# Kernel tuning notes

Measured on AMD Instinct MI355X. Metric: run time of the kernel, lower is better.

The kernel has to match this reference:

```python
import jax, jax.numpy as jnp
import numpy as np

NUM_EVENT, EVENT_DIM = 6, 32
NUM_WORD, WORD_DIM = 100000, 128
NUM_SKU, SKU_DIM = 500000, 128
NUM_CAT, CAT_DIM = 10000, 64
NUM_PRICE, PRICE_DIM = 100, 32
NUM_URL, URL_DIM = 200000, 128
HIDDEN = 512
B, S, W = 256, 256, 12
PAD = 0


def _table(key, n, d):
    t = jax.random.normal(key, (n, d), dtype=jnp.float32) * 0.02
    return t.at[PAD].set(0.0)  # padding_idx row is zero


def setup_inputs() -> dict:
    key = jax.random.key(0)
    ks = jax.random.split(key, 20)
    inp = {
        "event_table": _table(ks[0], NUM_EVENT, EVENT_DIM),
        "word_table": _table(ks[1], NUM_WORD, WORD_DIM),
        "sku_table": _table(ks[2], NUM_SKU, SKU_DIM),
        "cat_table": _table(ks[3], NUM_CAT, CAT_DIM),
        "price_table": _table(ks[4], NUM_PRICE, PRICE_DIM),
        "url_table": _table(ks[5], NUM_URL, URL_DIM),
        # Linear weights, torch convention: y = x @ W.T + b
        "sku_w": jax.random.normal(ks[6], (HIDDEN, EVENT_DIM + SKU_DIM + CAT_DIM + PRICE_DIM + WORD_DIM), dtype=jnp.float32) * 0.02,
        "sku_b": jnp.zeros((HIDDEN,), dtype=jnp.float32),
        "url_w": jax.random.normal(ks[7], (HIDDEN, URL_DIM + EVENT_DIM), dtype=jnp.float32) * 0.02,
        "url_b": jnp.zeros((HIDDEN,), dtype=jnp.float32),
        "query_w": jax.random.normal(ks[8], (HIDDEN, EVENT_DIM + WORD_DIM), dtype=jnp.float32) * 0.02,
        "query_b": jnp.zeros((HIDDEN,), dtype=jnp.float32),
        "event_type": jax.random.randint(ks[9], (B, S), 0, NUM_EVENT, dtype=jnp.int32),
        "sku_id": jax.random.randint(ks[10], (B, S), 0, NUM_SKU, dtype=jnp.int32),
        "url_id": jax.random.randint(ks[11], (B, S), 0, NUM_URL, dtype=jnp.int32),
        "cat_id": jax.random.randint(ks[12], (B, S), 0, NUM_CAT, dtype=jnp.int32),
        "price_id": jax.random.randint(ks[13], (B, S), 0, NUM_PRICE, dtype=jnp.int32),
        "word_id": jax.random.randint(ks[14], (B, S, W), 0, NUM_WORD, dtype=jnp.int32),
    }
    return inp


def _linear_relu(x, w, b):
    return jax.nn.relu(jnp.einsum("bsi,hi->bsh", x, w) + b)


def reference(event_table, word_table, sku_table, cat_table, price_table, url_table,
              sku_w, sku_b, url_w, url_b, query_w, query_b,
              event_type, sku_id, url_id, cat_id, price_id, word_id):
    # padding mask: 1.0 where event_type == PAD_IDX
    src_padding_mask = (event_type == PAD).astype(jnp.float32)

    event_emb = event_table[event_type]                 # [B,S,E]
    word_emb = word_table[word_id].mean(axis=-2)        # [B,S,Wd] (WordEmbedding avg)

    # SKU branch (event types 1,2,3): concat(event, sku, cat, price, word)
    sku_in = jnp.concatenate([event_emb, sku_table[sku_id], cat_table[cat_id],
                              price_table[price_id], word_emb], axis=-1)
    sku_out = _linear_relu(sku_in, sku_w, sku_b)        # [B,S,H]

    # URL branch (event type 4): concat(url, event)  -- note order in UrlEmbedding
    url_in = jnp.concatenate([url_table[url_id], event_emb], axis=-1)
    url_out = _linear_relu(url_in, url_w, url_b)

    # Query branch (event type 5): concat(event, word)
    query_in = jnp.concatenate([event_emb, word_emb], axis=-1)
    query_out = _linear_relu(query_in, query_w, query_b)

    is_sku = ((event_type >= 1) & (event_type <= 3))[..., None]
    is_url = (event_type == 4)[..., None]
    is_query = (event_type == 5)[..., None]

    seq_emb = (jnp.where(is_sku, sku_out, 0.0)
               + jnp.where(is_url, url_out, 0.0)
               + jnp.where(is_query, query_out, 0.0))   # PAD positions stay zero
    return seq_emb, src_padding_mask
```

## Files before the change

### kernel.cpp

```cpp
#include <hip/hip_runtime.h>
#include <hip/hip_bf16.h>
#if !__has_builtin(__builtin_amdgcn_cvt_pk_fp8_f32) || !__has_builtin(__builtin_amdgcn_cvt_pk_f32_fp8)
#include <hip/hip_fp8.h>
#endif

#define CUR_OFF   0
#define SLOT_OFF  1024
#define POS_OFF   263168
#define WSKU_OFF  1049600
#define WURL_OFF  1246208
#define WQRY_OFF  1344512
#define WF8_OFF   2097152
#define XS_OFF    16777216
#define XU_OFF    50331648
#define XQ_OFF    68157440

#define NPOS      65536
#define OUT_MASK  33554432
#define F8_SCALE  64.0f
#define INV4096   (1.0f / 4096.0f)

typedef __attribute__((ext_vector_type(4))) float f32x4;
typedef __attribute__((ext_vector_type(2))) float f32x2;
typedef __attribute__((ext_vector_type(2))) unsigned int u32x2;

__device__ __forceinline__ float2 ld2(const float* p) {
    return *reinterpret_cast<const float2*>(p);
}

__device__ __forceinline__ unsigned int pk2_f8(float a, float b) {
#if __has_builtin(__builtin_amdgcn_cvt_pk_fp8_f32)
    return __builtin_amdgcn_cvt_pk_fp8_f32(a, b, 0u, false);
#else
    __hip_fp8_e4m3 fa(a), fb(b);
    return (unsigned int)fa.__x | ((unsigned int)fb.__x << 8);
#endif
}
__device__ __forceinline__ unsigned int pk4_f8(float a, float b, float c, float d) {
#if __has_builtin(__builtin_amdgcn_cvt_pk_fp8_f32)
    unsigned int v = 0;
    v = __builtin_amdgcn_cvt_pk_fp8_f32(a, b, v, false);
    v = __builtin_amdgcn_cvt_pk_fp8_f32(c, d, v, true);
    return v;
#else
    return pk2_f8(a, b) | (pk2_f8(c, d) << 16);
#endif
}
__device__ __forceinline__ float2 upk2_f8(unsigned int u) {
#if __has_builtin(__builtin_amdgcn_cvt_pk_f32_fp8)
    f32x2 r = __builtin_amdgcn_cvt_pk_f32_fp8(u, false);
    return make_float2(r.x, r.y);
#else
    __hip_fp8_e4m3 fa, fb;
    fa.__x = (unsigned char)(u & 0xff);
    fb.__x = (unsigned char)((u >> 8) & 0xff);
    return make_float2((float)fa, (float)fb);
#endif
}
__device__ __forceinline__ void st_f8x2(unsigned char* d, float a, float b) {
    *reinterpret_cast<unsigned short*>(d) = (unsigned short)(pk2_f8(a, b) & 0xffffu);
}

#define AS1(p) ((const __attribute__((address_space(1))) void*)(p))
#define AS3(p) ((__attribute__((address_space(3))) void*)(p))

__global__ __launch_bounds__(256) void prep_k(const float* __restrict__ sw,
                                              const float* __restrict__ uw,
                                              const float* __restrict__ qw,
                                              const float* __restrict__ word_t,
                                              char* ws) {
    const int b = blockIdx.x, t = threadIdx.x;
    if (b < 6250) {
        size_t i = ((size_t)b * 256 + t) * 8;
        f32x4 v0 = *reinterpret_cast<const f32x4*>(word_t + i);
        f32x4 v1 = *reinterpret_cast<const f32x4*>(word_t + i + 4);
        u32x2 pk;
        pk.x = pk4_f8(v0.x * F8_SCALE, v0.y * F8_SCALE, v0.z * F8_SCALE, v0.w * F8_SCALE);
        pk.y = pk4_f8(v1.x * F8_SCALE, v1.y * F8_SCALE, v1.z * F8_SCALE, v1.w * F8_SCALE);
        *reinterpret_cast<u32x2*>((unsigned char*)(ws + WF8_OFF) + i) = pk;
        return;
    }
    int tt = (b - 6250) * 256 + t;
    if (tt < 3) ((int*)(ws + CUR_OFF))[tt] = 0;
    if (tt < 196608) {
        ((unsigned char*)(ws + WSKU_OFF))[tt] =
            (unsigned char)(pk2_f8(sw[tt] * F8_SCALE, 0.f) & 0xffu);
    } else if (tt < 294912) {
        int i = tt - 196608; int n = i / 192, k = i % 192;
        ((unsigned char*)(ws + WURL_OFF))[i] = (k < 160)
            ? (unsigned char)(pk2_f8(uw[n * 160 + k] * F8_SCALE, 0.f) & 0xffu) : 0;
    } else {
        int i = tt - 294912; int n = i / 192, k = i % 192;
        ((unsigned char*)(ws + WQRY_OFF))[i] = (k < 160)
            ? (unsigned char)(pk2_f8(qw[n * 160 + k] * F8_SCALE, 0.f) & 0xffu) : 0;
    }
}

__global__ __launch_bounds__(256) void alloc_k(const int* __restrict__ et_a,
                                               float* __restrict__ out, char* ws) {
    __shared__ int s_wcnt[4][3];
    __shared__ int s_base[3];
    __shared__ int s_woff[4][3];
    const int t = threadIdx.x, lane = t & 63, wid = t >> 6;
    int p = blockIdx.x * 256 + t;
    int et = et_a[p];
    int br = (et >= 1 && et <= 3) ? 0 : (et == 4 ? 1 : (et == 5 ? 2 : -1));
    unsigned long long m0 = __ballot(br == 0);
    unsigned long long m1 = __ballot(br == 1);
    unsigned long long m2 = __ballot(br == 2);
    if (lane == 0) {
        s_wcnt[wid][0] = (int)__popcll(m0);
        s_wcnt[wid][1] = (int)__popcll(m1);
        s_wcnt[wid][2] = (int)__popcll(m2);
    }
    __syncthreads();
    if (t < 3) {
        int c0 = s_wcnt[0][t], c1 = s_wcnt[1][t], c2 = s_wcnt[2][t], c3 = s_wcnt[3][t];
        int tot = c0 + c1 + c2 + c3;
        s_base[t] = tot ? atomicAdd(&((int*)(ws + CUR_OFF))[t], tot) : 0;
        s_woff[0][t] = 0; s_woff[1][t] = c0; s_woff[2][t] = c0 + c1; s_woff[3][t] = c0 + c1 + c2;
    }
    __syncthreads();
    unsigned long long lt = (1ull << lane) - 1ull;
    int slot = -1;
    if (br == 0)      slot = s_base[0] + s_woff[wid][0] + (int)__popcll(m0 & lt);
    else if (br == 1) slot = s_base[1] + s_woff[wid][1] + (int)__popcll(m1 & lt);
    else if (br == 2) slot = s_base[2] + s_woff[wid][2] + (int)__popcll(m2 & lt);
    ((int*)(ws + SLOT_OFF))[p] = slot;
    if (slot >= 0) ((int*)(ws + POS_OFF))[br * NPOS + slot] = p;
    __builtin_nontemporal_store((et == 0) ? 1.0f : 0.0f, &out[OUT_MASK + p]);
}

__device__ __forceinline__ float2 wsum_f8(const unsigned char* __restrict__ wt8,
                                          const int* __restrict__ wids, int lane) {
    float sx = 0.f, sy = 0.f;
    #pragma unroll
    for (int k = 0; k < 12; ++k) {
        unsigned int u = *reinterpret_cast<const unsigned short*>(
            wt8 + (size_t)wids[k] * 128 + 2 * lane);
        float2 v = upk2_f8(u);
        sx += v.x; sy += v.y;
    }
    const float inv = 1.0f / 12.0f;
    return make_float2(sx * inv, sy * inv);
}

__global__ __launch_bounds__(256) void build_k(
    const float* __restrict__ ev_t,
    const float* __restrict__ sku_t,  const float* __restrict__ cat_t,
    const float* __restrict__ price_t,const float* __restrict__ url_t,
    const int* __restrict__ et_a,     const int* __restrict__ sku_id,
    const int* __restrict__ url_id,   const int* __restrict__ cat_id,
    const int* __restrict__ price_id, const int* __restrict__ word_id,
    float* __restrict__ out, char* ws)
{
    const int t = threadIdx.x, lane = t & 63, wid = t >> 6;
    const int p = blockIdx.x * 4 + wid;
    const int et = et_a[p];
    if (et == 0) {
        f32x4 z = {0.f, 0.f, 0.f, 0.f};
        float* orow = out + (size_t)p * 512;
        __builtin_nontemporal_store(z, reinterpret_cast<f32x4*>(&orow[lane * 8]));
        __builtin_nontemporal_store(z, reinterpret_cast<f32x4*>(&orow[lane * 8 + 4]));
        return;
    }
    const int slot = ((const int*)(ws + SLOT_OFF))[p];
    const unsigned char* wf8 = (const unsigned char*)(ws + WF8_OFF);
    const float* evr = ev_t + et * 32;
    if (et <= 3) {
        unsigned char* X = (unsigned char*)(ws + XS_OFF) + (size_t)slot * 384;
        if (lane < 16) { float2 e = ld2(evr + 2 * lane);
                         st_f8x2(X + 2 * lane, e.x * F8_SCALE, e.y * F8_SCALE); }
        const float* sr = sku_t + (size_t)sku_id[p] * 128;
        { float2 s = ld2(sr + 2 * lane);
          st_f8x2(X + 32 + 2 * lane, s.x * F8_SCALE, s.y * F8_SCALE); }
        if (lane < 32) { const float* cr = cat_t + (size_t)cat_id[p] * 64;
                         float2 c = ld2(cr + 2 * lane);
                         st_f8x2(X + 160 + 2 * lane, c.x * F8_SCALE, c.y * F8_SCALE); }
        if (lane < 16) { const float* pr = price_t + (size_t)price_id[p] * 32;
                         float2 v = ld2(pr + 2 * lane);
                         st_f8x2(X + 224 + 2 * lane, v.x * F8_SCALE, v.y * F8_SCALE); }
        float2 w = wsum_f8(wf8, word_id + (size_t)p * 12, lane);
        st_f8x2(X + 256 + 2 * lane, w.x, w.y);
    } else if (et == 4) {
        unsigned char* X = (unsigned char*)(ws + XU_OFF) + (size_t)slot * 192;
        const float* ur = url_t + (size_t)url_id[p] * 128;
        { float2 u = ld2(ur + 2 * lane);
          st_f8x2(X + 2 * lane, u.x * F8_SCALE, u.y * F8_SCALE); }
        if (lane < 16) { float2 e = ld2(evr + 2 * lane);
                         st_f8x2(X + 128 + 2 * lane, e.x * F8_SCALE, e.y * F8_SCALE); }
        if (lane >= 48) *reinterpret_cast<unsigned short*>(X + 160 + 2 * (lane - 48)) = 0;
    } else {
        unsigned char* X = (unsigned char*)(ws + XQ_OFF) + (size_t)slot * 192;
        if (lane < 16) { float2 e = ld2(evr + 2 * lane);
                         st_f8x2(X + 2 * lane, e.x * F8_SCALE, e.y * F8_SCALE); }
        float2 w = wsum_f8(wf8, word_id + (size_t)p * 12, lane);
        st_f8x2(X + 32 + 2 * lane, w.x, w.y);
        if (lane >= 48) *reinterpret_cast<unsigned short*>(X + 160 + 2 * (lane - 48)) = 0;
    }
}

__global__ __launch_bounds__(256, 2) void gemm2_k(
    const char* __restrict__ ws_c, const float* __restrict__ sku_b,
    const float* __restrict__ url_b, const float* __restrict__ qry_b,
    float* __restrict__ out)
{
    const int z = blockIdx.z;
    const int count = ((const int*)(ws_c + CUR_OFF))[z];
    const int nmt = (count + 127) >> 7;
    const int orig = blockIdx.x;
    if (orig >= nmt) return;
    const int q8 = nmt >> 3, r8 = nmt & 7;
    const int xcd = orig & 7, idx = orig >> 3;
    const int mt = (xcd < r8 ? xcd * (q8 + 1) : r8 * (q8 + 1) + (xcd - r8) * q8) + idx;
    const int row0 = mt * 128;

    const int* posm = (const int*)(ws_c + POS_OFF) + z * NPOS;
    const char* arena; const char* Wb; const float* bias; int astride;
    if (z == 0)      { arena = ws_c + XS_OFF; Wb = ws_c + WSKU_OFF; bias = sku_b; astride = 384; }
    else if (z == 1) { arena = ws_c + XU_OFF; Wb = ws_c + WURL_OFF; bias = url_b; astride = 192; }
    else             { arena = ws_c + XQ_OFF; Wb = ws_c + WQRY_OFF; bias = qry_b; astride = 192; }

    __shared__ char ldsA[49152];
    __shared__ char ldsB[2][16384];

    const int t = threadIdx.x, lane = t & 63, wid = t >> 6;
    const int wr = wid >> 1, wc = wid & 1;
    const int r = lane & 15, q = lane >> 4;

    auto stageA_full = [&](int ktA, int koff) {
        #pragma unroll
        for (int i = 0; i < 4; ++i) {
            int row = i * 32 + (t >> 3);
            int sb  = (t & 7) ^ (row & 7);
            const char* ga = arena + (size_t)(row0 + row) * astride + koff + sb * 16;
            __builtin_amdgcn_global_load_lds(AS1(ga), AS3(&ldsA[ktA * 16384 + i * 4096 + t * 16]), 16, 0, 0);
        }
    };
    auto stageA_half = [&](int koff) {
        #pragma unroll
        for (int i = 0; i < 2; ++i) {
            int row = i * 64 + (t >> 2);
            int sb  = (t & 3) ^ (row & 3);
            const char* ga = arena + (size_t)(row0 + row) * astride + koff + sb * 16;
            __builtin_amdgcn_global_load_lds(AS1(ga), AS3(&ldsA[16384 + i * 4096 + t * 16]), 16, 0, 0);
        }
    };
    auto stageB_full = [&](int buf, int nc, int koff) {
        #pragma unroll
        for (int i = 0; i < 4; ++i) {
            int row = i * 32 + (t >> 3);
            int sb  = (t & 7) ^ (row & 7);
            const char* gb = Wb + (size_t)(nc * 128 + row) * astride + koff + sb * 16;
            __builtin_amdgcn_global_load_lds(AS1(gb), AS3(&ldsB[buf][i * 4096 + t * 16]), 16, 0, 0);
        }
    };
    auto stageB_half = [&](int buf, int nc, int koff) {
        #pragma unroll
        for (int i = 0; i < 2; ++i) {
            int row = i * 64 + (t >> 2);
            int sb  = (t & 3) ^ (row & 3);
            const char* gb = Wb + (size_t)(nc * 128 + row) * astride + koff + sb * 16;
            __builtin_amdgcn_global_load_lds(AS1(gb), AS3(&ldsB[buf][i * 4096 + t * 16]), 16, 0, 0);
        }
    };

    if (z == 0) { stageA_full(0, 0); stageA_full(1, 128); stageA_full(2, 256); }
    else        { stageA_full(0, 0); stageA_half(128); }
    stageB_full(0, 0, 0);
    if (z == 0) stageB_full(1, 0, 128); else stageB_half(1, 0, 128);
    __syncthreads();

    int posr[16];
    #pragma unroll
    for (int m = 0; m < 4; ++m)
        #pragma unroll
        for (int j = 0; j < 4; ++j) {
            int gr = row0 + wr * 64 + m * 16 + q * 4 + j;
            posr[m * 4 + j] = (gr < count) ? posm[gr] : -1;
        }

    f32x4 acc[4][4];
    auto compA_full = [&](int ktA, int buf) {
        #pragma unroll
        for (int kk = 0; kk < 4; ++kk) {
            const int u  = kk * 2 + (q >> 1);
            const int wo = (q & 1) * 8;
            long af[4], bf[4];
            #pragma unroll
            for (int m = 0; m < 4; ++m) {
                int arow = wr * 64 + m * 16 + r;
                af[m] = *reinterpret_cast<const long*>(
                    &ldsA[ktA * 16384 + arow * 128 + ((u ^ (arow & 7)) << 4) + wo]);
            }
            #pragma unroll
            for (int n = 0; n < 4; ++n) {
                int brow = wc * 64 + n * 16 + r;
                bf[n] = *reinterpret_cast<const long*>(
                    &ldsB[buf][brow * 128 + ((u ^ (brow & 7)) << 4) + wo]);
            }
            #pragma unroll
            for (int m = 0; m < 4; ++m)
                #pragma unroll
                for (int n = 0; n < 4; ++n)
                    acc[m][n] = __builtin_amdgcn_mfma_f32_16x16x32_fp8_fp8(af[m], bf[n], acc[m][n], 0, 0, 0);
        }
    };
    auto compA_half = [&](int buf) {
        #pragma unroll
        for (int kk = 0; kk < 2; ++kk) {
            const int u  = kk * 2 + (q >> 1);
            const int wo = (q & 1) * 8;
            long af[4], bf[4];
            #pragma unroll
            for (int m = 0; m < 4; ++m) {
                int arow = wr * 64 + m * 16 + r;
                af[m] = *reinterpret_cast<const long*>(
                    &ldsA[16384 + arow * 64 + ((u ^ (arow & 3)) << 4) + wo]);
            }
            #pragma unroll
            for (int n = 0; n < 4; ++n) {
                int brow = wc * 64 + n * 16 + r;
                bf[n] = *reinterpret_cast<const long*>(
                    &ldsB[buf][brow * 64 + ((u ^ (brow & 3)) << 4) + wo]);
            }
            #pragma unroll
            for (int m = 0; m < 4; ++m)
                #pragma unroll
                for (int n = 0; n < 4; ++n)
                    acc[m][n] = __builtin_amdgcn_mfma_f32_16x16x32_fp8_fp8(af[m], bf[n], acc[m][n], 0, 0, 0);
        }
    };
    auto epilogue = [&](int nc) {
        float bv[4];
        #pragma unroll
        for (int n = 0; n < 4; ++n) bv[n] = bias[nc * 128 + wc * 64 + n * 16 + r];
        #pragma unroll
        for (int m = 0; m < 4; ++m)
            #pragma unroll
            for (int j = 0; j < 4; ++j) {
                int pos = posr[m * 4 + j];
                if (pos >= 0) {
                    float* orow = out + (size_t)pos * 512 + nc * 128 + wc * 64;
                    #pragma unroll
                    for (int n = 0; n < 4; ++n)
                        __builtin_nontemporal_store(
                            fmaxf(acc[m][n][j] * INV4096 + bv[n], 0.f), &orow[n * 16 + r]);
                }
            }
    };

    if (z == 0) {
        for (int nc = 0; nc < 4; ++nc) {
            #pragma unroll
            for (int m = 0; m < 4; ++m)
                #pragma unroll
                for (int n = 0; n < 4; ++n)
                    acc[m][n] = (f32x4){0.f, 0.f, 0.f, 0.f};
            #pragma unroll
            for (int kt = 0; kt < 3; ++kt) {
                int j = nc * 3 + kt, jn = j + 1;
                if (jn < 12) stageB_full(jn & 1, jn / 3, (jn % 3) * 128);
                compA_full(kt, j & 1);
                __syncthreads();
            }
            epilogue(nc);
        }
    } else {
        for (int nc = 0; nc < 4; ++nc) {
            #pragma unroll
            for (int m = 0; m < 4; ++m)
                #pragma unroll
                for (int n = 0; n < 4; ++n)
                    acc[m][n] = (f32x4){0.f, 0.f, 0.f, 0.f};
            #pragma unroll
            for (int kt = 0; kt < 2; ++kt) {
                int j = nc * 2 + kt, jn = j + 1;
                if (jn < 8) {
                    if ((jn & 1) == 0) stageB_full(jn & 1, jn / 2, 0);
                    else               stageB_half(jn & 1, jn / 2, 128);
                }
                if (kt == 0) compA_full(0, j & 1);
                else         compA_half(j & 1);
                __syncthreads();
            }
            epilogue(nc);
        }
    }
}

extern "C" void kernel_launch(void* const* d_in, const int* in_sizes, int n_in,
                              void* d_out, int out_size, void* d_ws, size_t ws_size,
                              hipStream_t stream) {
    const float* ev_t    = (const float*)d_in[0];
    const float* word_t  = (const float*)d_in[1];
    const float* sku_t   = (const float*)d_in[2];
    const float* cat_t   = (const float*)d_in[3];
    const float* price_t = (const float*)d_in[4];
    const float* url_t   = (const float*)d_in[5];
    const float* sku_w   = (const float*)d_in[6];
    const float* sku_b   = (const float*)d_in[7];
    const float* url_w   = (const float*)d_in[8];
    const float* url_b   = (const float*)d_in[9];
    const float* query_w = (const float*)d_in[10];
    const float* query_b = (const float*)d_in[11];
    const int* event_type = (const int*)d_in[12];
    const int* sku_id     = (const int*)d_in[13];
    const int* url_id     = (const int*)d_in[14];
    const int* cat_id     = (const int*)d_in[15];
    const int* price_id   = (const int*)d_in[16];
    const int* word_id    = (const int*)d_in[17];

    char*  ws  = (char*)d_ws;
    float* out = (float*)d_out;

    prep_k<<<7786, 256, 0, stream>>>(sku_w, url_w, query_w, word_t, ws);
    alloc_k<<<256, 256, 0, stream>>>(event_type, out, ws);
    build_k<<<16384, 256, 0, stream>>>(ev_t, sku_t, cat_t, price_t, url_t,
                                       event_type, sku_id, url_id, cat_id, price_id,
                                       word_id, out, ws);
    dim3 gg(512, 1, 3);
    gemm2_k<<<gg, 256, 0, stream>>>(ws, sku_b, url_b, query_b, out);
}
```

Measured before the change: 87.00 us.

## Restructure gather kernel per branch with 16 lanes per row and wide loads

Result: faster. 76.39 us, median of 2 (-12.2%).

```diff
diff --git a/kernel.cpp b/kernel.cpp
--- a/kernel.cpp
+++ b/kernel.cpp
@@ -55,6 +55,14 @@
     fa.__x = (unsigned char)(u & 0xff);
     fb.__x = (unsigned char)((u >> 8) & 0xff);
     return make_float2((float)fa, (float)fb);
+#endif
+}
+__device__ __forceinline__ float2 upk2_f8_hi(unsigned int u) {
+#if __has_builtin(__builtin_amdgcn_cvt_pk_f32_fp8)
+    f32x2 r = __builtin_amdgcn_cvt_pk_f32_fp8(u, true);
+    return make_float2(r.x, r.y);
+#else
+    return upk2_f8(u >> 16);
 #endif
 }
 __device__ __forceinline__ void st_f8x2(unsigned char* d, float a, float b) {
@@ -101,9 +109,12 @@
     __shared__ int s_wcnt[4][3];
     __shared__ int s_base[3];
     __shared__ int s_woff[4][3];
+    __shared__ int s_et[256];
     const int t = threadIdx.x, lane = t & 63, wid = t >> 6;
-    int p = blockIdx.x * 256 + t;
+    const int p0 = blockIdx.x * 256;
+    int p = p0 + t;
     int et = et_a[p];
+    s_et[t] = et;
     int br = (et >= 1 && et <= 3) ? 0 : (et == 4 ? 1 : (et == 5 ? 2 : -1));
     unsigned long long m0 = __ballot(br == 0);
     unsigned long long m1 = __ballot(br == 1);
@@ -126,23 +137,30 @@
     if (br == 0)      slot = s_base[0] + s_woff[wid][0] + (int)__popcll(m0 & lt);
     else if (br == 1) slot = s_base[1] + s_woff[wid][1] + (int)__popcll(m1 & lt);
     else if (br == 2) slot = s_base[2] + s_woff[wid][2] + (int)__popcll(m2 & lt);
-    ((int*)(ws + SLOT_OFF))[p] = slot;
     if (slot >= 0) ((int*)(ws + POS_OFF))[br * NPOS + slot] = p;
     __builtin_nontemporal_store((et == 0) ? 1.0f : 0.0f, &out[OUT_MASK + p]);
-}
-
-__device__ __forceinline__ float2 wsum_f8(const unsigned char* __restrict__ wt8,
-                                          const int* __restrict__ wids, int lane) {
-    float sx = 0.f, sy = 0.f;
+    for (int i = wid; i < 256; i += 4) {
+        if (s_et[i] == 0) {
+            float* orow = out + (size_t)(p0 + i) * 512;
+            f32x4 z = {0.f, 0.f, 0.f, 0.f};
+            __builtin_nontemporal_store(z, reinterpret_cast<f32x4*>(&orow[lane * 8]));
+            __builtin_nontemporal_store(z, reinterpret_cast<f32x4*>(&orow[lane * 8 + 4]));
+        }
+    }
+}
+
+__device__ __forceinline__ void wsum8_f8(const unsigned char* __restrict__ wt8,
+                                         const int* __restrict__ wid_p, int l,
+                                         float* s) {
     #pragma unroll
     for (int k = 0; k < 12; ++k) {
-        unsigned int u = *reinterpret_cast<const unsigned short*>(
-            wt8 + (size_t)wids[k] * 128 + 2 * lane);
-        float2 v = upk2_f8(u);
-        sx += v.x; sy += v.y;
-    }
-    const float inv = 1.0f / 12.0f;
-    return make_float2(sx * inv, sy * inv);
+        int w = wid_p[k];
+        u32x2 u = *reinterpret_cast<const u32x2*>(wt8 + (size_t)w * 128 + 8 * l);
+        float2 a0 = upk2_f8(u.x), a1 = upk2_f8_hi(u.x);
+        float2 b0 = upk2_f8(u.y), b1 = upk2_f8_hi(u.y);
+        s[0] += a0.x; s[1] += a0.y; s[2] += a1.x; s[3] += a1.y;
+        s[4] += b0.x; s[5] += b0.y; s[6] += b1.x; s[7] += b1.y;
+    }
 }
 
 __global__ __launch_bounds__(256) void build_k(
@@ -152,51 +170,66 @@
     const int* __restrict__ et_a,     const int* __restrict__ sku_id,
     const int* __restrict__ url_id,   const int* __restrict__ cat_id,
     const int* __restrict__ price_id, const int* __restrict__ word_id,
-    float* __restrict__ out, char* ws)
+    char* ws)
 {
+    const int z = blockIdx.z;
+    const int count = ((const int*)(ws + CUR_OFF))[z];
+    const int slot0 = blockIdx.x * 16;
+    if (slot0 >= count) return;
     const int t = threadIdx.x, lane = t & 63, wid = t >> 6;
-    const int p = blockIdx.x * 4 + wid;
-    const int et = et_a[p];
-    if (et == 0) {
-        f32x4 z = {0.f, 0.f, 0.f, 0.f};
-        float* orow = out + (size_t)p * 512;
-        __builtin_nontemporal_store(z, reinterpret_cast<f32x4*>(&orow[lane * 8]));
-        __builtin_nontemporal_store(z, reinterpret_cast<f32x4*>(&orow[lane * 8 + 4]));
-        return;
-    }
-    const int slot = ((const int*)(ws + SLOT_OFF))[p];
+    const int g = lane >> 4, l = lane & 15;
+    const int slot = slot0 + wid * 4 + g;
+    if (slot >= count) return;
+    const int p = ((const int*)(ws + POS_OFF))[z * NPOS + slot];
     const unsigned char* wf8 = (const unsigned char*)(ws + WF8_OFF);
-    const float* evr = ev_t + et * 32;
-    if (et <= 3) {
+    const float inv = 1.0f / 12.0f;
+
+    if (z == 0) {
         unsigned char* X = (unsigned char*)(ws + XS_OFF) + (size_t)slot * 384;
-        if (lane < 16) { float2 e = ld2(evr + 2 * lane);
-                         st_f8x2(X + 2 * lane, e.x * F8_SCALE, e.y * F8_SCALE); }
-        const float* sr = sku_t + (size_t)sku_id[p] * 128;
-        { float2 s = ld2(sr + 2 * lane);
-          st_f8x2(X + 32 + 2 * lane, s.x * F8_SCALE, s.y * F8_SCALE); }
-        if (lane < 32) { const float* cr = cat_t + (size_t)cat_id[p] * 64;
-                         float2 c = ld2(cr + 2 * lane);
-                         st_f8x2(X + 160 + 2 * lane, c.x * F8_SCALE, c.y * F8_SCALE); }
-        if (lane < 16) { const float* pr = price_t + (size_t)price_id[p] * 32;
-                         float2 v = ld2(pr + 2 * lane);
-                         st_f8x2(X + 224 + 2 * lane, v.x * F8_SCALE, v.y * F8_SCALE); }
-        float2 w = wsum_f8(wf8, word_id + (size_t)p * 12, lane);
-        st_f8x2(X + 256 + 2 * lane, w.x, w.y);
-    } else if (et == 4) {
+        const int et = et_a[p];
+        float2 e = ld2(ev_t + et * 32 + 2 * l);
+        st_f8x2(X + 2 * l, e.x * F8_SCALE, e.y * F8_SCALE);
+        const float* sr = sku_t + (size_t)sku_id[p] * 128 + 8 * l;
+        f32x4 s0 = *reinterpret_cast<const f32x4*>(sr);
+        f32x4 s1 = *reinterpret_cast<const f32x4*>(sr + 4);
+        u32x2 sp;
+        sp.x = pk4_f8(s0.x * F8_SCALE, s0.y * F8_SCALE, s0.z * F8_SCALE, s0.w * F8_SCALE);
+        sp.y = pk4_f8(s1.x * F8_SCALE, s1.y * F8_SCALE, s1.z * F8_SCALE, s1.w * F8_SCALE);
+        *reinterpret_cast<u32x2*>(X + 32 + 8 * l) = sp;
+        f32x4 c = *reinterpret_cast<const f32x4*>(cat_t + (size_t)cat_id[p] * 64 + 4 * l);
+        *reinterpret_cast<unsigned int*>(X + 160 + 4 * l) =
+            pk4_f8(c.x * F8_SCALE, c.y * F8_SCALE, c.z * F8_SCALE, c.w * F8_SCALE);
+        float2 v = ld2(price_t + (size_t)price_id[p] * 32 + 2 * l);
+        st_f8x2(X + 224 + 2 * l, v.x * F8_SCALE, v.y * F8_SCALE);
+        float s[8] = {0.f, 0.f, 0.f, 0.f, 0.f, 0.f, 0.f, 0.f};
+        wsum8_f8(wf8, word_id + (size_t)p * 12, l, s);
+        u32x2 wp;
+        wp.x = pk4_f8(s[0] * inv, s[1] * inv, s[2] * inv, s[3] * inv);
+        wp.y = pk4_f8(s[4] * inv, s[5] * inv, s[6] * inv, s[7] * inv);
+        *reinterpret_cast<u32x2*>(X + 256 + 8 * l) = wp;
+    } else if (z == 1) {
         unsigned char* X = (unsigned char*)(ws + XU_OFF) + (size_t)slot * 192;
-        const float* ur = url_t + (size_t)url_id[p] * 128;
-        { float2 u = ld2(ur + 2 * lane);
-          st_f8x2(X + 2 * lane, u.x * F8_SCALE, u.y * F8_SCALE); }
-        if (lane < 16) { float2 e = ld2(evr + 2 * lane);
-                         st_f8x2(X + 128 + 2 * lane, e.x * F8_SCALE, e.y * F8_SCALE); }
-        if (lane >= 48) *reinterpret_cast<unsigned short*>(X + 160 + 2 * (lane - 48)) = 0;
+        const float* ur = url_t + (size_t)url_id[p] * 128 + 8 * l;
+        f32x4 u0 = *reinterpret_cast<const f32x4*>(ur);
+        f32x4 u1 = *reinterpret_cast<const f32x4*>(ur + 4);
+        u32x2 up;
+        up.x = pk4_f8(u0.x * F8_SCALE, u0.y * F8_SCALE, u0.z * F8_SCALE, u0.w * F8_SCALE);
+        up.y = pk4_f8(u1.x * F8_SCALE, u1.y * F8_SCALE, u1.z * F8_SCALE, u1.w * F8_SCALE);
+        *reinterpret_cast<u32x2*>(X + 8 * l) = up;
+        float2 e = ld2(ev_t + 4 * 32 + 2 * l);
+        st_f8x2(X + 128 + 2 * l, e.x * F8_SCALE, e.y * F8_SCALE);
+        *reinterpret_cast<unsigned short*>(X + 160 + 2 * l) = 0;
     } else {
         unsigned char* X = (unsigned char*)(ws + XQ_OFF) + (size_t)slot * 192;
-        if (lane < 16) { float2 e = ld2(evr + 2 * lane);
-                         st_f8x2(X + 2 * lane, e.x * F8_SCALE, e.y * F8_SCALE); }
-        float2 w = wsum_f8(wf8, word_id + (size_t)p * 12, lane);
-        st_f8x2(X + 32 + 2 * lane, w.x, w.y);
-        if (lane >= 48) *reinterpret_cast<unsigned short*>(X + 160 + 2 * (lane - 48)) = 0;
+        float2 e = ld2(ev_t + 5 * 32 + 2 * l);
+        st_f8x2(X + 2 * l, e.x * F8_SCALE, e.y * F8_SCALE);
+        float s[8] = {0.f, 0.f, 0.f, 0.f, 0.f, 0.f, 0.f, 0.f};
+        wsum8_f8(wf8, word_id + (size_t)p * 12, l, s);
+        u32x2 wp;
+        wp.x = pk4_f8(s[0] * inv, s[1] * inv, s[2] * inv, s[3] * inv);
+        wp.y = pk4_f8(s[4] * inv, s[5] * inv, s[6] * inv, s[7] * inv);
+        *reinterpret_cast<u32x2*>(X + 32 + 8 * l) = wp;
+        *reinterpret_cast<unsigned short*>(X + 160 + 2 * l) = 0;
     }
 }
 
@@ -416,9 +449,10 @@
 
     prep_k<<<7786, 256, 0, stream>>>(sku_w, url_w, query_w, word_t, ws);
     alloc_k<<<256, 256, 0, stream>>>(event_type, out, ws);
-    build_k<<<16384, 256, 0, stream>>>(ev_t, sku_t, cat_t, price_t, url_t,
-                                       event_type, sku_id, url_id, cat_id, price_id,
-                                       word_id, out, ws);
+    dim3 gb(4096, 1, 3);
+    build_k<<<gb, 256, 0, stream>>>(ev_t, sku_t, cat_t, price_t, url_t,
+                                    event_type, sku_id, url_id, cat_id, price_id,
+                                    word_id, ws);
     dim3 gg(512, 1, 3);
     gemm2_k<<<gg, 256, 0, stream>>>(ws, sku_b, url_b, query_b, out);
 }
```
